# Optimization experiments

Hardware: AMD Instinct MI355X
Metric: run time of the kernel (lower is better)

Reference implementation:

```python
import jax, jax.numpy as jnp
import numpy as np

T, D, I, E, K = 2048, 768, 2048, 8, 2


def setup_inputs() -> dict:
    key = jax.random.key(0)
    ks = jax.random.split(key, 9)
    x = jax.random.normal(ks[0], (T, D), jnp.float32)
    router_weight = jax.random.normal(ks[1], (E, D), jnp.float32) * 0.02
    shared_w_gate = jax.random.normal(ks[2], (I, D), jnp.float32) * 0.02
    shared_w_up = jax.random.normal(ks[3], (I, D), jnp.float32) * 0.02
    shared_w_down = jax.random.normal(ks[4], (D, I), jnp.float32) * 0.02
    # ternary quantized expert weights in {-1, 0, 1}
    expert_q_gate = jax.random.randint(ks[5], (E, I, D), 0, 3, jnp.int32) - 1
    expert_q_up = jax.random.randint(ks[6], (E, I, D), 0, 3, jnp.int32) - 1
    expert_q_down = jax.random.randint(ks[7], (E, D, I), 0, 3, jnp.int32) - 1
    # per-expert, per-matrix dequant scales (gate, up, down)
    expert_scales = jax.random.uniform(ks[8], (E, 3), jnp.float32) * 0.05 + 0.01
    return {
        "x": x,
        "router_weight": router_weight,
        "shared_w_gate": shared_w_gate,
        "shared_w_up": shared_w_up,
        "shared_w_down": shared_w_down,
        "expert_q_gate": expert_q_gate,
        "expert_q_up": expert_q_up,
        "expert_q_down": expert_q_down,
        "expert_scales": expert_scales,
        "top_k": K,
    }


def _swiglu(x, wg, wu, wd):
    # down( silu(gate(x)) * up(x) )
    return (jax.nn.silu(x @ wg.T) * (x @ wu.T)) @ wd.T


def reference(x, router_weight, shared_w_gate, shared_w_up, shared_w_down,
              expert_q_gate, expert_q_up, expert_q_down, expert_scales, top_k):
    # --- router: softmax -> top-k -> renormalize ---
    probs = jax.nn.softmax(x @ router_weight.T, axis=-1)            # [T, E]
    vals, idx = jax.lax.top_k(probs, top_k)                          # [T, K]
    vals = vals / jnp.sum(vals, axis=-1, keepdims=True)
    n_experts = router_weight.shape[0]
    # combine weights as dense [T, E] gate (one-hot scatter of top-k probs)
    gate = jnp.sum(jax.nn.one_hot(idx, n_experts, dtype=x.dtype) * vals[..., None], axis=1)

    # --- dequantize paged ternary experts: w = ternary * scale ---
    wg = expert_q_gate.astype(x.dtype) * expert_scales[:, 0, None, None]  # [E, I, D]
    wu = expert_q_up.astype(x.dtype) * expert_scales[:, 1, None, None]    # [E, I, D]
    wd = expert_q_down.astype(x.dtype) * expert_scales[:, 2, None, None]  # [E, D, I]

    # --- expert SwiGLU, computed per expert and combined with the gate ---
    h = jax.nn.silu(jnp.einsum('td,eid->tei', x, wg)) * jnp.einsum('td,eid->tei', x, wu)
    expert_out = jnp.einsum('tei,edi->ted', h, wd)                   # [T, E, D]
    moe_out = jnp.einsum('te,ted->td', gate, expert_out)             # [T, D]

    # --- always-on shared expert ---
    shared_out = _swiglu(x, shared_w_gate, shared_w_up, shared_w_down)
    return shared_out + moe_out
```

## Files before the change

### kernel.cpp

```cpp
#include <hip/hip_runtime.h>
#include <hip/hip_bf16.h>

#define TDIM 2048
#define DDIM 768
#define IDIM 2048
#define NEXP 8

typedef __bf16 v8bf __attribute__((ext_vector_type(8)));
typedef __bf16 v4bf __attribute__((ext_vector_type(4)));
typedef float v4f __attribute__((ext_vector_type(4)));
typedef int   v4i __attribute__((ext_vector_type(4)));
typedef float v4ff __attribute__((ext_vector_type(4)));

#define MFMA_B16(A,B,C) __builtin_amdgcn_mfma_f32_16x16x32_bf16(A,B,C,0,0,0)

typedef __attribute__((address_space(1))) const unsigned int* gas_t;
typedef __attribute__((address_space(3))) unsigned int* las_t;

__device__ __forceinline__ void gload16(const void* g, void* l) {
  __builtin_amdgcn_global_load_lds((gas_t)g, (las_t)l, 16, 0, 0);
}

__device__ __forceinline__ v4bf cvt4_i(v4i a) {
  v4bf v;
  v[0] = (__bf16)(float)a[0]; v[1] = (__bf16)(float)a[1];
  v[2] = (__bf16)(float)a[2]; v[3] = (__bf16)(float)a[3];
  return v;
}
__device__ __forceinline__ v4bf cvt4_f(v4ff a) {
  v4bf v;
  v[0] = (__bf16)a[0]; v[1] = (__bf16)a[1]; v[2] = (__bf16)a[2]; v[3] = (__bf16)a[3];
  return v;
}

__global__ __launch_bounds__(256)
void pack_all_kernel(const int* __restrict__ qg, const int* __restrict__ qu,
                     const int* __restrict__ qd,
                     const float* __restrict__ sg, const float* __restrict__ su,
                     const float* __restrict__ sd, const float* __restrict__ x,
                     const float* __restrict__ rw, const float* __restrict__ es,
                     __hip_bfloat16* __restrict__ wguT, __hip_bfloat16* __restrict__ sguT,
                     __hip_bfloat16* __restrict__ wdT,  __hip_bfloat16* __restrict__ sdT,
                     __hip_bfloat16* __restrict__ xb,
                     int* __restrict__ cnt, int* __restrict__ lists, float* __restrict__ wt)
{
  const int b = blockIdx.x;
  const int tid = threadIdx.x;

  if (b < 512) {
    const int t = b * 4 + (tid >> 6);
    const int lane = tid & 63;
    const float* xp = x + (size_t)t * DDIM;
    float4 xv0 = *(const float4*)(xp + lane * 4);
    float4 xv1 = *(const float4*)(xp + 256 + lane * 4);
    float4 xv2 = *(const float4*)(xp + 512 + lane * 4);
    float logit[NEXP];
#pragma unroll
    for (int e = 0; e < NEXP; ++e) {
      const float* w = rw + (size_t)e * DDIM;
      float4 w0 = *(const float4*)(w + lane * 4);
      float4 w1 = *(const float4*)(w + 256 + lane * 4);
      float4 w2 = *(const float4*)(w + 512 + lane * 4);
      float p = xv0.x * w0.x + xv0.y * w0.y + xv0.z * w0.z + xv0.w * w0.w
              + xv1.x * w1.x + xv1.y * w1.y + xv1.z * w1.z + xv1.w * w1.w
              + xv2.x * w2.x + xv2.y * w2.y + xv2.z * w2.z + xv2.w * w2.w;
#pragma unroll
      for (int off = 32; off > 0; off >>= 1) p += __shfl_down(p, off, 64);
      logit[e] = p;
    }
    if (lane == 0) {
      float m = logit[0];
#pragma unroll
      for (int e = 1; e < NEXP; ++e) m = fmaxf(m, logit[e]);
      float pr[NEXP];
#pragma unroll
      for (int e = 0; e < NEXP; ++e) pr[e] = expf(logit[e] - m);
      int i0 = 0; float v0 = pr[0];
#pragma unroll
      for (int e = 1; e < NEXP; ++e) if (pr[e] > v0) { v0 = pr[e]; i0 = e; }
      int i1 = -1; float v1 = -1.f;
#pragma unroll
      for (int e = 0; e < NEXP; ++e) if (e != i0 && pr[e] > v1) { v1 = pr[e]; i1 = e; }
      float inv = 1.f / (v0 + v1);
      int p0 = atomicAdd(&cnt[i0], 1);
      lists[i0 * TDIM + p0] = t * 2;
      wt[t * 2] = v0 * inv * es[i0 * 3 + 2];
      int p1 = atomicAdd(&cnt[i1], 1);
      lists[i1 * TDIM + p1] = t * 2 + 1;
      wt[t * 2 + 1] = v1 * inv * es[i1 * 3 + 2];
    }
    return;
  }

  const int lc = tid & 31;
  const int rowloc = tid >> 5;

  if (b < 768) {
    const int row = (b - 512) * 8 + rowloc;
    const float* sp = x + (size_t)row * DDIM;
    __hip_bfloat16* dp = xb + (size_t)row * DDIM;
    v4ff r[6];
#pragma unroll
    for (int i = 0; i < 6; ++i) r[i] = *(const v4ff*)(sp + (lc + i * 32) * 4);
#pragma unroll
    for (int i = 0; i < 6; ++i) *(v4bf*)(dp + (lc + i * 32) * 4) = cvt4_f(r[i]);
    return;
  }

  if (b < 5376) {
    const int pb = b - 768;
    const int* isrc = nullptr; const float* fsrc = nullptr;
    char* dstT; int T, r8, isint;
    if (pb < 4096) {
      const int e = pb >> 9; T = (pb >> 8) & 1; r8 = pb & 255;
      isrc = (T ? qu : qg) + (size_t)e * IDIM * DDIM;
      dstT = (char*)wguT + (size_t)e * 32 * 12 * 16384;
      isint = 1;
    } else {
      const int sb = pb - 4096; T = sb >> 8; r8 = sb & 255;
      fsrc = T ? su : sg;
      dstT = (char*)sguT;
      isint = 0;
    }
    const int srcrow = r8 * 8 + rowloc;
    const int rg = ((srcrow >> 4) * 32) + (srcrow & 15) + T * 16;
    const int tnt = rg >> 7, rowin = rg & 127;
    const int xorm = (rowin & 7) << 4;
    char* rowdst = dstT + (size_t)tnt * (12 * 16384) + rowin * 128;
    const size_t soff = (size_t)srcrow * DDIM;

    if (isint) {
      v4i r[6];
#pragma unroll
      for (int i = 0; i < 6; ++i) r[i] = *(const v4i*)(isrc + soff + (lc + i * 32) * 4);
#pragma unroll
      for (int i = 0; i < 6; ++i) {
        const int c4 = lc + i * 32;
        const int kt = c4 >> 4;
        *(v4bf*)(rowdst + (size_t)kt * 16384 + (((c4 & 15) << 3) ^ xorm)) = cvt4_i(r[i]);
      }
    } else {
      v4ff r[6];
#pragma unroll
      for (int i = 0; i < 6; ++i) r[i] = *(const v4ff*)(fsrc + soff + (lc + i * 32) * 4);
#pragma unroll
      for (int i = 0; i < 6; ++i) {
        const int c4 = lc + i * 32;
        const int kt = c4 >> 4;
        *(v4bf*)(rowdst + (size_t)kt * 16384 + (((c4 & 15) << 3) ^ xorm)) = cvt4_f(r[i]);
      }
    }
    return;
  }

  {
    const int pb = b - 5376;
    const int* isrc = nullptr; const float* fsrc = nullptr;
    char* dstT; int r8, isint;
    if (pb < 768) {
      const int e = pb / 96; r8 = pb % 96;
      isrc = qd + (size_t)e * DDIM * IDIM;
      dstT = (char*)wdT + (size_t)e * (192 * 16384);
      isint = 1;
    } else {
      r8 = pb - 768;
      fsrc = sd;
      dstT = (char*)sdT;
      isint = 0;
    }
    const int srcrow = r8 * 8 + rowloc;
    const int tnt = srcrow >> 7, rowin = srcrow & 127;
    const int xorm = (rowin & 7) << 4;
    char* rowdst = dstT + (size_t)tnt * (32 * 16384) + rowin * 128;
    const size_t soff = (size_t)srcrow * IDIM;

#pragma unroll
    for (int h = 0; h < 2; ++h) {
      if (isint) {
        v4i r[8];
#pragma unroll
        for (int j = 0; j < 8; ++j) r[j] = *(const v4i*)(isrc + soff + (lc + (h * 8 + j) * 32) * 4);
#pragma unroll
        for (int j = 0; j < 8; ++j) {
          const int c4 = lc + (h * 8 + j) * 32;
          const int kt = c4 >> 4;
          *(v4bf*)(rowdst + (size_t)kt * 16384 + (((c4 & 15) << 3) ^ xorm)) = cvt4_i(r[j]);
        }
      } else {
        v4ff r[8];
#pragma unroll
        for (int j = 0; j < 8; ++j) r[j] = *(const v4ff*)(fsrc + soff + (lc + (h * 8 + j) * 32) * 4);
#pragma unroll
        for (int j = 0; j < 8; ++j) {
          const int c4 = lc + (h * 8 + j) * 32;
          const int kt = c4 >> 4;
          *(v4bf*)(rowdst + (size_t)kt * 16384 + (((c4 & 15) << 3) ^ xorm)) = cvt4_f(r[j]);
        }
      }
    }
  }
}

__global__ __launch_bounds__(256, 3)
void gu_gemm_kernel(const __hip_bfloat16* __restrict__ xb,
                    const __hip_bfloat16* __restrict__ wguT, const __hip_bfloat16* __restrict__ sguT,
                    const float* __restrict__ es,
                    const int* __restrict__ cnt, const int* __restrict__ lists,
                    __hip_bfloat16* __restrict__ h)
{
  const int b = blockIdx.x;
  int tm, tn, count;
  const char* bbase;
  const int* listE = nullptr;
  float sgc, suc;
  if (b < 4096) {
    const int e = b >> 9; tm = (b >> 5) & 15; tn = b & 31;
    count = cnt[e];
    if (tm * 128 >= count) return;
    bbase = (const char*)wguT + (size_t)(e * 32 + tn) * (12 * 16384);
    listE = lists + e * TDIM;
    sgc = es[e * 3 + 0]; suc = es[e * 3 + 1];
  } else {
    const int b2 = b - 4096; tm = b2 >> 5; tn = b2 & 31;
    count = TDIM;
    bbase = (const char*)sguT + (size_t)tn * (12 * 16384);
    sgc = 1.f; suc = 1.f;
  }

  __shared__ __align__(16) char As[16384];
  __shared__ __align__(16) char Bs[16384];

  const int tid = threadIdx.x;
  const int lane = tid & 63;
  const int wid = tid >> 6;
  const int wr = wid >> 1, wc = wid & 1;
  const int lr16 = lane & 15, hk = lane >> 4;

  const int cA = (((lane & 7) ^ (lane >> 3)) << 4);
  const char* aptr[4];
#pragma unroll
  for (int p = 0; p < 4; ++p) {
    const int row = p * 32 + wid * 8 + (lane >> 3);
    const int rg = tm * 128 + row;
    int tok;
    if (listE) { const int idx = rg < count ? rg : count - 1; tok = listE[idx] >> 1; }
    else tok = rg;
    aptr[p] = (const char*)xb + (size_t)tok * (DDIM * 2) + cA;
  }
  const char* bp = bbase + wid * 1024 + lane * 16;

  v4f acc[4][4] = {};

  for (int kt = 0; kt < 12; ++kt) {
#pragma unroll
    for (int p = 0; p < 4; ++p) gload16(aptr[p] + kt * 128, As + wid * 1024 + p * 4096);
#pragma unroll
    for (int p = 0; p < 4; ++p) gload16(bp + kt * 16384 + p * 4096, Bs + wid * 1024 + p * 4096);
    __syncthreads();
#pragma unroll
    for (int ks = 0; ks < 2; ++ks) {
      const int colb = ks * 64 + hk * 16;
      v8bf fa[4], fb[4];
#pragma unroll
      for (int m = 0; m < 4; ++m) {
        const int r = wr * 64 + m * 16 + lr16;
        fa[m] = *(const v8bf*)(As + r * 128 + (colb ^ ((r & 7) << 4)));
      }
#pragma unroll
      for (int n = 0; n < 4; ++n) {
        const int r = wc * 64 + n * 16 + lr16;
        fb[n] = *(const v8bf*)(Bs + r * 128 + (colb ^ ((r & 7) << 4)));
      }
#pragma unroll
      for (int n = 0; n < 4; ++n)
#pragma unroll
        for (int m = 0; m < 4; ++m) acc[m][n] = MFMA_B16(fa[m], fb[n], acc[m][n]);
    }
    __syncthreads();
  }

#pragma unroll
  for (int m = 0; m < 4; ++m) {
#pragma unroll
    for (int j = 0; j < 4; ++j) {
      const int rl = wr * 64 + m * 16 + hk * 4 + j;
      const int rg = tm * 128 + rl;
      if (rg >= count) continue;
      const size_t drow = listE ? (size_t)listE[rg] : (size_t)(4096 + rg);
      __hip_bfloat16* dh = h + drow * IDIM + (tn * 4 + wc * 2) * 16 + lr16;
#pragma unroll
      for (int p = 0; p < 2; ++p) {
        const float g = acc[m][2 * p][j] * sgc;
        const float u = acc[m][2 * p + 1][j] * suc;
        dh[p * 16] = __float2bfloat16(g / (1.f + __expf(-g)) * u);
      }
    }
  }
}

__global__ __launch_bounds__(256, 3)
void down_kernel(const __hip_bfloat16* __restrict__ h,
                 const __hip_bfloat16* __restrict__ wdT, const __hip_bfloat16* __restrict__ sdT,
                 const float* __restrict__ wt,
                 const int* __restrict__ cnt, const int* __restrict__ lists,
                 float* __restrict__ out)
{
  const int b = blockIdx.x;
  int tm, tn, count;
  const char* bbase;
  const int* listE = nullptr;
  if (b < 768) {
    const int e = b / 96; const int r = b % 96; tm = r / 6; tn = r % 6;
    count = cnt[e];
    if (tm * 128 >= count) return;
    bbase = (const char*)wdT + (size_t)(e * 6 + tn) * (32 * 16384);
    listE = lists + e * TDIM;
  } else {
    const int r = b - 768; tm = r / 6; tn = r % 6;
    count = TDIM;
    bbase = (const char*)sdT + (size_t)tn * (32 * 16384);
  }

  __shared__ __align__(16) char As[16384];
  __shared__ __align__(16) char Bs[16384];

  const int tid = threadIdx.x;
  const int lane = tid & 63;
  const int wid = tid >> 6;
  const int wr = wid >> 1, wc = wid & 1;
  const int lr16 = lane & 15, hk = lane >> 4;

  const int cA = (((lane & 7) ^ (lane >> 3)) << 4);
  const char* aptr[4];
#pragma unroll
  for (int p = 0; p < 4; ++p) {
    const int row = p * 32 + wid * 8 + (lane >> 3);
    const int rg = tm * 128 + row;
    int srow;
    if (listE) { const int idx = rg < count ? rg : count - 1; srow = listE[idx]; }
    else srow = 4096 + rg;
    aptr[p] = (const char*)h + (size_t)srow * (IDIM * 2) + cA;
  }
  const char* bp = bbase + wid * 1024 + lane * 16;

  v4f acc[4][4] = {};

  for (int kt = 0; kt < 32; ++kt) {
#pragma unroll
    for (int p = 0; p < 4; ++p) gload16(aptr[p] + kt * 128, As + wid * 1024 + p * 4096);
#pragma unroll
    for (int p = 0; p < 4; ++p) gload16(bp + kt * 16384 + p * 4096, Bs + wid * 1024 + p * 4096);
    __syncthreads();
#pragma unroll
    for (int ks = 0; ks < 2; ++ks) {
      const int colb = ks * 64 + hk * 16;
      v8bf fa[4], fb[4];
#pragma unroll
      for (int m = 0; m < 4; ++m) {
        const int r = wr * 64 + m * 16 + lr16;
        fa[m] = *(const v8bf*)(As + r * 128 + (colb ^ ((r & 7) << 4)));
      }
#pragma unroll
      for (int n = 0; n < 4; ++n) {
        const int r = wc * 64 + n * 16 + lr16;
        fb[n] = *(const v8bf*)(Bs + r * 128 + (colb ^ ((r & 7) << 4)));
      }
#pragma unroll
      for (int n = 0; n < 4; ++n)
#pragma unroll
        for (int m = 0; m < 4; ++m) acc[m][n] = MFMA_B16(fa[m], fb[n], acc[m][n]);
    }
    __syncthreads();
  }

#pragma unroll
  for (int m = 0; m < 4; ++m) {
#pragma unroll
    for (int j = 0; j < 4; ++j) {
      const int rl = wr * 64 + m * 16 + hk * 4 + j;
      const int rg = tm * 128 + rl;
      if (rg >= count) continue;
      int tok; float w;
      if (listE) { const int slot = listE[rg]; tok = slot >> 1; w = wt[slot]; }
      else { tok = rg; w = 1.f; }
      float* dst = out + (size_t)tok * DDIM + tn * 128 + wc * 64 + lr16;
#pragma unroll
      for (int n = 0; n < 4; ++n) atomicAdd(dst + n * 16, acc[m][n][j] * w);
    }
  }
}

extern "C" void kernel_launch(void* const* d_in, const int* in_sizes, int n_in,
                              void* d_out, int out_size, void* d_ws, size_t ws_size,
                              hipStream_t stream)
{
  const float* x   = (const float*)d_in[0];
  const float* rw  = (const float*)d_in[1];
  const float* swg = (const float*)d_in[2];
  const float* swu = (const float*)d_in[3];
  const float* swd = (const float*)d_in[4];
  const int*   qg  = (const int*)d_in[5];
  const int*   qu  = (const int*)d_in[6];
  const int*   qd  = (const int*)d_in[7];
  const float* es  = (const float*)d_in[8];
  float* out = (float*)d_out;

  char* ws = (char*)d_ws;
  size_t off = 0;
  auto alloc = [&](size_t bytes) { void* p = ws + off; off = (off + bytes + 255) & ~(size_t)255; return p; };
  int*   cnt   = (int*)alloc(NEXP * 4);
  int*   lists = (int*)alloc((size_t)NEXP * TDIM * 4);
  float* wt    = (float*)alloc((size_t)2 * TDIM * 4);
  __hip_bfloat16* xb   = (__hip_bfloat16*)alloc((size_t)TDIM * DDIM * 2);
  __hip_bfloat16* wguT = (__hip_bfloat16*)alloc((size_t)NEXP * 32 * 12 * 8192 * 2);
  __hip_bfloat16* sguT = (__hip_bfloat16*)alloc((size_t)32 * 12 * 8192 * 2);
  __hip_bfloat16* wdT  = (__hip_bfloat16*)alloc((size_t)NEXP * 6 * 32 * 8192 * 2);
  __hip_bfloat16* sdT  = (__hip_bfloat16*)alloc((size_t)6 * 32 * 8192 * 2);
  __hip_bfloat16* h    = (__hip_bfloat16*)alloc((size_t)(4096 + TDIM) * IDIM * 2);

  hipMemsetAsync(cnt, 0, NEXP * 4, stream);
  hipMemsetAsync(out, 0, (size_t)TDIM * DDIM * 4, stream);

  pack_all_kernel<<<6240, 256, 0, stream>>>(qg, qu, qd, swg, swu, swd, x, rw, es,
                                            wguT, sguT, wdT, sdT, xb, cnt, lists, wt);
  gu_gemm_kernel<<<4096 + 512, 256, 0, stream>>>(xb, wguT, sguT, es, cnt, lists, h);
  down_kernel<<<768 + 96, 256, 0, stream>>>(h, wdT, sdT, wt, cnt, lists, out);
}
```

Baseline: 351.4 us.

## Fuse weight dequantization into GEMM loads and replace atomics with combine pass

Drops the separate pack pass that converted int32 ternary and fp32 shared weights into pre-swizzled bf16 buffers. The GEMM kernels now read the raw weights, convert them in registers and store them to LDS, with register prefetch and a double-buffered A tile. The down kernel writes per-slot partial outputs rather than doing atomicAdd into out, and a new combine kernel sums the two expert partials and the shared partial for each token. This avoids a large write and re-read of packed weights, but each GEMM tile now re-reads 4-byte weights (twice the bf16 bytes) and does the conversion every time, and the combine pass adds extra traffic.

```diff
diff --git a/kernel.cpp b/kernel.cpp
--- a/kernel.cpp
+++ b/kernel.cpp
@@ -21,28 +21,22 @@
   __builtin_amdgcn_global_load_lds((gas_t)g, (las_t)l, 16, 0, 0);
 }
 
-__device__ __forceinline__ v4bf cvt4_i(v4i a) {
+__device__ __forceinline__ v4bf conv4(v4i r, int isint) {
   v4bf v;
-  v[0] = (__bf16)(float)a[0]; v[1] = (__bf16)(float)a[1];
-  v[2] = (__bf16)(float)a[2]; v[3] = (__bf16)(float)a[3];
+  if (isint) {
+    v[0] = (__bf16)(float)r[0]; v[1] = (__bf16)(float)r[1];
+    v[2] = (__bf16)(float)r[2]; v[3] = (__bf16)(float)r[3];
+  } else {
+    v[0] = (__bf16)__int_as_float(r[0]); v[1] = (__bf16)__int_as_float(r[1]);
+    v[2] = (__bf16)__int_as_float(r[2]); v[3] = (__bf16)__int_as_float(r[3]);
+  }
   return v;
 }
-__device__ __forceinline__ v4bf cvt4_f(v4ff a) {
-  v4bf v;
-  v[0] = (__bf16)a[0]; v[1] = (__bf16)a[1]; v[2] = (__bf16)a[2]; v[3] = (__bf16)a[3];
-  return v;
-}
 
 __global__ __launch_bounds__(256)
-void pack_all_kernel(const int* __restrict__ qg, const int* __restrict__ qu,
-                     const int* __restrict__ qd,
-                     const float* __restrict__ sg, const float* __restrict__ su,
-                     const float* __restrict__ sd, const float* __restrict__ x,
-                     const float* __restrict__ rw, const float* __restrict__ es,
-                     __hip_bfloat16* __restrict__ wguT, __hip_bfloat16* __restrict__ sguT,
-                     __hip_bfloat16* __restrict__ wdT,  __hip_bfloat16* __restrict__ sdT,
-                     __hip_bfloat16* __restrict__ xb,
-                     int* __restrict__ cnt, int* __restrict__ lists, float* __restrict__ wt)
+void prep_kernel(const float* __restrict__ x, const float* __restrict__ rw,
+                 const float* __restrict__ es, __hip_bfloat16* __restrict__ xb,
+                 int* __restrict__ cnt, int* __restrict__ lists, float* __restrict__ wt)
 {
   const int b = blockIdx.x;
   const int tid = threadIdx.x;
@@ -94,140 +88,51 @@
 
   const int lc = tid & 31;
   const int rowloc = tid >> 5;
-
-  if (b < 768) {
-    const int row = (b - 512) * 8 + rowloc;
-    const float* sp = x + (size_t)row * DDIM;
-    __hip_bfloat16* dp = xb + (size_t)row * DDIM;
-    v4ff r[6];
-#pragma unroll
-    for (int i = 0; i < 6; ++i) r[i] = *(const v4ff*)(sp + (lc + i * 32) * 4);
-#pragma unroll
-    for (int i = 0; i < 6; ++i) *(v4bf*)(dp + (lc + i * 32) * 4) = cvt4_f(r[i]);
-    return;
-  }
-
-  if (b < 5376) {
-    const int pb = b - 768;
-    const int* isrc = nullptr; const float* fsrc = nullptr;
-    char* dstT; int T, r8, isint;
-    if (pb < 4096) {
-      const int e = pb >> 9; T = (pb >> 8) & 1; r8 = pb & 255;
-      isrc = (T ? qu : qg) + (size_t)e * IDIM * DDIM;
-      dstT = (char*)wguT + (size_t)e * 32 * 12 * 16384;
-      isint = 1;
-    } else {
-      const int sb = pb - 4096; T = sb >> 8; r8 = sb & 255;
-      fsrc = T ? su : sg;
-      dstT = (char*)sguT;
-      isint = 0;
-    }
-    const int srcrow = r8 * 8 + rowloc;
-    const int rg = ((srcrow >> 4) * 32) + (srcrow & 15) + T * 16;
-    const int tnt = rg >> 7, rowin = rg & 127;
-    const int xorm = (rowin & 7) << 4;
-    char* rowdst = dstT + (size_t)tnt * (12 * 16384) + rowin * 128;
-    const size_t soff = (size_t)srcrow * DDIM;
-
-    if (isint) {
-      v4i r[6];
-#pragma unroll
-      for (int i = 0; i < 6; ++i) r[i] = *(const v4i*)(isrc + soff + (lc + i * 32) * 4);
-#pragma unroll
-      for (int i = 0; i < 6; ++i) {
-        const int c4 = lc + i * 32;
-        const int kt = c4 >> 4;
-        *(v4bf*)(rowdst + (size_t)kt * 16384 + (((c4 & 15) << 3) ^ xorm)) = cvt4_i(r[i]);
-      }
-    } else {
-      v4ff r[6];
-#pragma unroll
-      for (int i = 0; i < 6; ++i) r[i] = *(const v4ff*)(fsrc + soff + (lc + i * 32) * 4);
-#pragma unroll
-      for (int i = 0; i < 6; ++i) {
-        const int c4 = lc + i * 32;
-        const int kt = c4 >> 4;
-        *(v4bf*)(rowdst + (size_t)kt * 16384 + (((c4 & 15) << 3) ^ xorm)) = cvt4_f(r[i]);
-      }
-    }
-    return;
-  }
-
-  {
-    const int pb = b - 5376;
-    const int* isrc = nullptr; const float* fsrc = nullptr;
-    char* dstT; int r8, isint;
-    if (pb < 768) {
-      const int e = pb / 96; r8 = pb % 96;
-      isrc = qd + (size_t)e * DDIM * IDIM;
-      dstT = (char*)wdT + (size_t)e * (192 * 16384);
-      isint = 1;
-    } else {
-      r8 = pb - 768;
-      fsrc = sd;
-      dstT = (char*)sdT;
-      isint = 0;
-    }
-    const int srcrow = r8 * 8 + rowloc;
-    const int tnt = srcrow >> 7, rowin = srcrow & 127;
-    const int xorm = (rowin & 7) << 4;
-    char* rowdst = dstT + (size_t)tnt * (32 * 16384) + rowin * 128;
-    const size_t soff = (size_t)srcrow * IDIM;
-
-#pragma unroll
-    for (int h = 0; h < 2; ++h) {
-      if (isint) {
-        v4i r[8];
-#pragma unroll
-        for (int j = 0; j < 8; ++j) r[j] = *(const v4i*)(isrc + soff + (lc + (h * 8 + j) * 32) * 4);
-#pragma unroll
-        for (int j = 0; j < 8; ++j) {
-          const int c4 = lc + (h * 8 + j) * 32;
-          const int kt = c4 >> 4;
-          *(v4bf*)(rowdst + (size_t)kt * 16384 + (((c4 & 15) << 3) ^ xorm)) = cvt4_i(r[j]);
-        }
-      } else {
-        v4ff r[8];
-#pragma unroll
-        for (int j = 0; j < 8; ++j) r[j] = *(const v4ff*)(fsrc + soff + (lc + (h * 8 + j) * 32) * 4);
-#pragma unroll
-        for (int j = 0; j < 8; ++j) {
-          const int c4 = lc + (h * 8 + j) * 32;
-          const int kt = c4 >> 4;
-          *(v4bf*)(rowdst + (size_t)kt * 16384 + (((c4 & 15) << 3) ^ xorm)) = cvt4_f(r[j]);
-        }
-      }
-    }
-  }
-}
-
-__global__ __launch_bounds__(256, 3)
+  const int row = (b - 512) * 8 + rowloc;
+  const float* sp = x + (size_t)row * DDIM;
+  __hip_bfloat16* dp = xb + (size_t)row * DDIM;
+  v4ff r[6];
+#pragma unroll
+  for (int i = 0; i < 6; ++i) r[i] = *(const v4ff*)(sp + (lc + i * 32) * 4);
+#pragma unroll
+  for (int i = 0; i < 6; ++i) {
+    v4bf v;
+    v[0] = (__bf16)r[i][0]; v[1] = (__bf16)r[i][1];
+    v[2] = (__bf16)r[i][2]; v[3] = (__bf16)r[i][3];
+    *(v4bf*)(dp + (lc + i * 32) * 4) = v;
+  }
+}
+
+__global__ __launch_bounds__(256)
 void gu_gemm_kernel(const __hip_bfloat16* __restrict__ xb,
-                    const __hip_bfloat16* __restrict__ wguT, const __hip_bfloat16* __restrict__ sguT,
+                    const int* __restrict__ qg, const int* __restrict__ qu,
+                    const float* __restrict__ sgw, const float* __restrict__ suw,
                     const float* __restrict__ es,
                     const int* __restrict__ cnt, const int* __restrict__ lists,
                     __hip_bfloat16* __restrict__ h)
 {
   const int b = blockIdx.x;
-  int tm, tn, count;
-  const char* bbase;
+  int tm, tn, count, isint;
+  const char *srcG, *srcU;
   const int* listE = nullptr;
   float sgc, suc;
   if (b < 4096) {
     const int e = b >> 9; tm = (b >> 5) & 15; tn = b & 31;
     count = cnt[e];
     if (tm * 128 >= count) return;
-    bbase = (const char*)wguT + (size_t)(e * 32 + tn) * (12 * 16384);
+    srcG = (const char*)(qg + (size_t)e * IDIM * DDIM);
+    srcU = (const char*)(qu + (size_t)e * IDIM * DDIM);
     listE = lists + e * TDIM;
     sgc = es[e * 3 + 0]; suc = es[e * 3 + 1];
+    isint = 1;
   } else {
     const int b2 = b - 4096; tm = b2 >> 5; tn = b2 & 31;
     count = TDIM;
-    bbase = (const char*)sguT + (size_t)tn * (12 * 16384);
-    sgc = 1.f; suc = 1.f;
-  }
-
-  __shared__ __align__(16) char As[16384];
+    srcG = (const char*)sgw; srcU = (const char*)suw;
+    sgc = 1.f; suc = 1.f; isint = 0;
+  }
+
+  __shared__ __align__(16) char As[2][16384];
   __shared__ __align__(16) char Bs[16384];
 
   const int tid = threadIdx.x;
@@ -247,16 +152,42 @@
     else tok = rg;
     aptr[p] = (const char*)xb + (size_t)tok * (DDIM * 2) + cA;
   }
-  const char* bp = bbase + wid * 1024 + lane * 16;
+
+  const int lanec = tid & 15;
+  const int rowb = tid >> 4;
+  const char* bq[8];
+  int dsoff[8];
+#pragma unroll
+  for (int p = 0; p < 8; ++p) {
+    const int srcrow = (tn * 4 + (p >> 1)) * 16 + rowb;
+    const char* base = (p & 1) ? srcU : srcG;
+    bq[p] = base + ((size_t)srcrow * DDIM + lanec * 4) * 4;
+    const int r = rowb + 16 * p;
+    dsoff[p] = r * 128 + ((lanec * 8) ^ ((rowb & 7) << 4));
+  }
 
   v4f acc[4][4] = {};
+  v4i braw[8];
+  v4bf bconv[8];
+
+#pragma unroll
+  for (int p = 0; p < 4; ++p) gload16(aptr[p], As[0] + wid * 1024 + p * 4096);
+#pragma unroll
+  for (int p = 0; p < 8; ++p) braw[p] = *(const v4i*)(bq[p]);
+#pragma unroll
+  for (int p = 0; p < 8; ++p) bconv[p] = conv4(braw[p], isint);
 
   for (int kt = 0; kt < 12; ++kt) {
-#pragma unroll
-    for (int p = 0; p < 4; ++p) gload16(aptr[p] + kt * 128, As + wid * 1024 + p * 4096);
-#pragma unroll
-    for (int p = 0; p < 4; ++p) gload16(bp + kt * 16384 + p * 4096, Bs + wid * 1024 + p * 4096);
+    const int cur = kt & 1;
+#pragma unroll
+    for (int p = 0; p < 8; ++p) *(v4bf*)(Bs + dsoff[p]) = bconv[p];
     __syncthreads();
+    if (kt + 1 < 12) {
+#pragma unroll
+      for (int p = 0; p < 4; ++p) gload16(aptr[p] + (kt + 1) * 128, As[cur ^ 1] + wid * 1024 + p * 4096);
+#pragma unroll
+      for (int p = 0; p < 8; ++p) braw[p] = *(const v4i*)(bq[p] + (kt + 1) * 256);
+    }
 #pragma unroll
     for (int ks = 0; ks < 2; ++ks) {
       const int colb = ks * 64 + hk * 16;
@@ -264,7 +195,7 @@
 #pragma unroll
       for (int m = 0; m < 4; ++m) {
         const int r = wr * 64 + m * 16 + lr16;
-        fa[m] = *(const v8bf*)(As + r * 128 + (colb ^ ((r & 7) << 4)));
+        fa[m] = *(const v8bf*)(As[cur] + r * 128 + (colb ^ ((r & 7) << 4)));
       }
 #pragma unroll
       for (int n = 0; n < 4; ++n) {
@@ -277,6 +208,10 @@
         for (int m = 0; m < 4; ++m) acc[m][n] = MFMA_B16(fa[m], fb[n], acc[m][n]);
     }
     __syncthreads();
+    if (kt + 1 < 12) {
+#pragma unroll
+      for (int p = 0; p < 8; ++p) bconv[p] = conv4(braw[p], isint);
+    }
   }
 
 #pragma unroll
@@ -298,30 +233,32 @@
   }
 }
 
-__global__ __launch_bounds__(256, 3)
-void down_kernel(const __hip_bfloat16* __restrict__ h,
-                 const __hip_bfloat16* __restrict__ wdT, const __hip_bfloat16* __restrict__ sdT,
-                 const float* __restrict__ wt,
-                 const int* __restrict__ cnt, const int* __restrict__ lists,
-                 float* __restrict__ out)
+__global__ __launch_bounds__(256)
+void down_gemm_kernel(const __hip_bfloat16* __restrict__ h,
+                      const int* __restrict__ qd, const float* __restrict__ sdw,
+                      const float* __restrict__ wt,
+                      const int* __restrict__ cnt, const int* __restrict__ lists,
+                      float* __restrict__ part)
 {
   const int b = blockIdx.x;
-  int tm, tn, count;
-  const char* bbase;
+  int tm, tn, count, isint;
+  const char* srcB;
   const int* listE = nullptr;
   if (b < 768) {
     const int e = b / 96; const int r = b % 96; tm = r / 6; tn = r % 6;
     count = cnt[e];
     if (tm * 128 >= count) return;
-    bbase = (const char*)wdT + (size_t)(e * 6 + tn) * (32 * 16384);
+    srcB = (const char*)(qd + (size_t)e * DDIM * IDIM);
     listE = lists + e * TDIM;
+    isint = 1;
   } else {
     const int r = b - 768; tm = r / 6; tn = r % 6;
     count = TDIM;
-    bbase = (const char*)sdT + (size_t)tn * (32 * 16384);
-  }
-
-  __shared__ __align__(16) char As[16384];
+    srcB = (const char*)sdw;
+    isint = 0;
+  }
+
+  __shared__ __align__(16) char As[2][16384];
   __shared__ __align__(16) char Bs[16384];
 
   const int tid = threadIdx.x;
@@ -341,16 +278,41 @@
     else srow = 4096 + rg;
     aptr[p] = (const char*)h + (size_t)srow * (IDIM * 2) + cA;
   }
-  const char* bp = bbase + wid * 1024 + lane * 16;
+
+  const int lanec = tid & 15;
+  const int rowb = tid >> 4;
+  const char* bq[8];
+  int dsoff[8];
+#pragma unroll
+  for (int p = 0; p < 8; ++p) {
+    const int srcrow = tn * 128 + rowb + 16 * p;
+    bq[p] = srcB + ((size_t)srcrow * IDIM + lanec * 4) * 4;
+    const int r = rowb + 16 * p;
+    dsoff[p] = r * 128 + ((lanec * 8) ^ ((rowb & 7) << 4));
+  }
 
   v4f acc[4][4] = {};
+  v4i braw[8];
+  v4bf bconv[8];
+
+#pragma unroll
+  for (int p = 0; p < 4; ++p) gload16(aptr[p], As[0] + wid * 1024 + p * 4096);
+#pragma unroll
+  for (int p = 0; p < 8; ++p) braw[p] = *(const v4i*)(bq[p]);
+#pragma unroll
+  for (int p = 0; p < 8; ++p) bconv[p] = conv4(braw[p], isint);
 
   for (int kt = 0; kt < 32; ++kt) {
-#pragma unroll
-    for (int p = 0; p < 4; ++p) gload16(aptr[p] + kt * 128, As + wid * 1024 + p * 4096);
-#pragma unroll
-    for (int p = 0; p < 4; ++p) gload16(bp + kt * 16384 + p * 4096, Bs + wid * 1024 + p * 4096);
+    const int cur = kt & 1;
+#pragma unroll
+    for (int p = 0; p < 8; ++p) *(v4bf*)(Bs + dsoff[p]) = bconv[p];
     __syncthreads();
+    if (kt + 1 < 32) {
+#pragma unroll
+      for (int p = 0; p < 4; ++p) gload16(aptr[p] + (kt + 1) * 128, As[cur ^ 1] + wid * 1024 + p * 4096);
+#pragma unroll
+      for (int p = 0; p < 8; ++p) braw[p] = *(const v4i*)(bq[p] + (kt + 1) * 256);
+    }
 #pragma unroll
     for (int ks = 0; ks < 2; ++ks) {
       const int colb = ks * 64 + hk * 16;
@@ -358,7 +320,7 @@
 #pragma unroll
       for (int m = 0; m < 4; ++m) {
         const int r = wr * 64 + m * 16 + lr16;
-        fa[m] = *(const v8bf*)(As + r * 128 + (colb ^ ((r & 7) << 4)));
+        fa[m] = *(const v8bf*)(As[cur] + r * 128 + (colb ^ ((r & 7) << 4)));
       }
 #pragma unroll
       for (int n = 0; n < 4; ++n) {
@@ -371,6 +333,10 @@
         for (int m = 0; m < 4; ++m) acc[m][n] = MFMA_B16(fa[m], fb[n], acc[m][n]);
     }
     __syncthreads();
+    if (kt + 1 < 32) {
+#pragma unroll
+      for (int p = 0; p < 8; ++p) bconv[p] = conv4(braw[p], isint);
+    }
   }
 
 #pragma unroll
@@ -380,14 +346,32 @@
       const int rl = wr * 64 + m * 16 + hk * 4 + j;
       const int rg = tm * 128 + rl;
       if (rg >= count) continue;
-      int tok; float w;
-      if (listE) { const int slot = listE[rg]; tok = slot >> 1; w = wt[slot]; }
-      else { tok = rg; w = 1.f; }
-      float* dst = out + (size_t)tok * DDIM + tn * 128 + wc * 64 + lr16;
-#pragma unroll
-      for (int n = 0; n < 4; ++n) atomicAdd(dst + n * 16, acc[m][n][j] * w);
-    }
-  }
+      int orow; float w;
+      if (listE) { const int slot = listE[rg]; orow = slot; w = wt[slot]; }
+      else { orow = 4096 + rg; w = 1.f; }
+      float* dst = part + (size_t)orow * DDIM + tn * 128 + wc * 64 + lr16;
+#pragma unroll
+      for (int n = 0; n < 4; ++n) dst[n * 16] = acc[m][n][j] * w;
+    }
+  }
+}
+
+__global__ __launch_bounds__(256)
+void combine_kernel(const float* __restrict__ part, float* __restrict__ out)
+{
+  const int i4 = blockIdx.x * 256 + threadIdx.x;
+  const int i0 = i4 * 4;
+  const int t = i0 / DDIM;
+  const int d = i0 - t * DDIM;
+  float4 a = *(const float4*)(part + (size_t)(2 * t) * DDIM + d);
+  float4 bb = *(const float4*)(part + (size_t)(2 * t + 1) * DDIM + d);
+  float4 c = *(const float4*)(part + (size_t)(4096 + t) * DDIM + d);
+  float4 r;
+  r.x = a.x + bb.x + c.x;
+  r.y = a.y + bb.y + c.y;
+  r.z = a.z + bb.z + c.z;
+  r.w = a.w + bb.w + c.w;
+  *(float4*)(out + i0) = r;
 }
 
 extern "C" void kernel_launch(void* const* d_in, const int* in_sizes, int n_in,
@@ -411,18 +395,14 @@
   int*   cnt   = (int*)alloc(NEXP * 4);
   int*   lists = (int*)alloc((size_t)NEXP * TDIM * 4);
   float* wt    = (float*)alloc((size_t)2 * TDIM * 4);
-  __hip_bfloat16* xb   = (__hip_bfloat16*)alloc((size_t)TDIM * DDIM * 2);
-  __hip_bfloat16* wguT = (__hip_bfloat16*)alloc((size_t)NEXP * 32 * 12 * 8192 * 2);
-  __hip_bfloat16* sguT = (__hip_bfloat16*)alloc((size_t)32 * 12 * 8192 * 2);
-  __hip_bfloat16* wdT  = (__hip_bfloat16*)alloc((size_t)NEXP * 6 * 32 * 8192 * 2);
-  __hip_bfloat16* sdT  = (__hip_bfloat16*)alloc((size_t)6 * 32 * 8192 * 2);
-  __hip_bfloat16* h    = (__hip_bfloat16*)alloc((size_t)(4096 + TDIM) * IDIM * 2);
+  __hip_bfloat16* xb = (__hip_bfloat16*)alloc((size_t)TDIM * DDIM * 2);
+  __hip_bfloat16* h  = (__hip_bfloat16*)alloc((size_t)(4096 + TDIM) * IDIM * 2);
+  float* part = (float*)alloc((size_t)(4096 + TDIM) * DDIM * 4);
 
   hipMemsetAsync(cnt, 0, NEXP * 4, stream);
-  hipMemsetAsync(out, 0, (size_t)TDIM * DDIM * 4, stream);
-
-  pack_all_kernel<<<6240, 256, 0, stream>>>(qg, qu, qd, swg, swu, swd, x, rw, es,
-                                            wguT, sguT, wdT, sdT, xb, cnt, lists, wt);
-  gu_gemm_kernel<<<4096 + 512, 256, 0, stream>>>(xb, wguT, sguT, es, cnt, lists, h);
-  down_kernel<<<768 + 96, 256, 0, stream>>>(h, wdT, sdT, wt, cnt, lists, out);
-}
+
+  prep_kernel<<<768, 256, 0, stream>>>(x, rw, es, xb, cnt, lists, wt);
+  gu_gemm_kernel<<<4096 + 512, 256, 0, stream>>>(xb, qg, qu, swg, swu, es, cnt, lists, h);
+  down_gemm_kernel<<<768 + 96, 256, 0, stream>>>(h, qd, swd, wt, cnt, lists, part);
+  combine_kernel<<<(TDIM * DDIM / 4) / 256, 256, 0, stream>>>(part, out);
+}
```

Result: slower. 389.1 us (+10.7%).

## Store packed weights row-major and replace down atomics with partials plus combine

Applied to the files above, without the earlier changes.

The weight packing now writes plain row-major bf16 rows instead of pre-swizzled tile blocks. The GEMMs gather B rows with per-row pointers and an XOR column offset, which moves the swizzle from the pack stores to the load side. The down GEMM no longer does float atomicAdd into the output. It writes per-slot partial rows into a scratch buffer, and a new combine kernel sums the two expert slots and the shared row per token. This removes atomic contention and the output memset, at the cost of an extra kernel, extra scratch traffic, and strided B loads that are less contiguous.

```diff
diff --git a/kernel.cpp b/kernel.cpp
--- a/kernel.cpp
+++ b/kernel.cpp
@@ -39,8 +39,8 @@
                      const float* __restrict__ sg, const float* __restrict__ su,
                      const float* __restrict__ sd, const float* __restrict__ x,
                      const float* __restrict__ rw, const float* __restrict__ es,
-                     __hip_bfloat16* __restrict__ wguT, __hip_bfloat16* __restrict__ sguT,
-                     __hip_bfloat16* __restrict__ wdT,  __hip_bfloat16* __restrict__ sdT,
+                     __hip_bfloat16* __restrict__ wgub, __hip_bfloat16* __restrict__ sgub,
+                     __hip_bfloat16* __restrict__ wdb,  __hip_bfloat16* __restrict__ sdb,
                      __hip_bfloat16* __restrict__ xb,
                      int* __restrict__ cnt, int* __restrict__ lists, float* __restrict__ wt)
 {
@@ -110,45 +110,36 @@
   if (b < 5376) {
     const int pb = b - 768;
     const int* isrc = nullptr; const float* fsrc = nullptr;
-    char* dstT; int T, r8, isint;
+    __hip_bfloat16* dstT; int T, r8, isint;
     if (pb < 4096) {
       const int e = pb >> 9; T = (pb >> 8) & 1; r8 = pb & 255;
       isrc = (T ? qu : qg) + (size_t)e * IDIM * DDIM;
-      dstT = (char*)wguT + (size_t)e * 32 * 12 * 16384;
+      dstT = wgub + (size_t)e * (2 * IDIM) * DDIM;
       isint = 1;
     } else {
       const int sb = pb - 4096; T = sb >> 8; r8 = sb & 255;
       fsrc = T ? su : sg;
-      dstT = (char*)sguT;
+      dstT = sgub;
       isint = 0;
     }
     const int srcrow = r8 * 8 + rowloc;
     const int rg = ((srcrow >> 4) * 32) + (srcrow & 15) + T * 16;
-    const int tnt = rg >> 7, rowin = rg & 127;
-    const int xorm = (rowin & 7) << 4;
-    char* rowdst = dstT + (size_t)tnt * (12 * 16384) + rowin * 128;
-    const size_t soff = (size_t)srcrow * DDIM;
+    __hip_bfloat16* dp = dstT + (size_t)rg * DDIM;
 
     if (isint) {
+      const v4i* sp = (const v4i*)(isrc + (size_t)srcrow * DDIM);
       v4i r[6];
 #pragma unroll
-      for (int i = 0; i < 6; ++i) r[i] = *(const v4i*)(isrc + soff + (lc + i * 32) * 4);
-#pragma unroll
-      for (int i = 0; i < 6; ++i) {
-        const int c4 = lc + i * 32;
-        const int kt = c4 >> 4;
-        *(v4bf*)(rowdst + (size_t)kt * 16384 + (((c4 & 15) << 3) ^ xorm)) = cvt4_i(r[i]);
-      }
+      for (int i = 0; i < 6; ++i) r[i] = sp[lc + i * 32];
+#pragma unroll
+      for (int i = 0; i < 6; ++i) *(v4bf*)(dp + (lc + i * 32) * 4) = cvt4_i(r[i]);
     } else {
+      const v4ff* sp = (const v4ff*)(fsrc + (size_t)srcrow * DDIM);
       v4ff r[6];
 #pragma unroll
-      for (int i = 0; i < 6; ++i) r[i] = *(const v4ff*)(fsrc + soff + (lc + i * 32) * 4);
-#pragma unroll
-      for (int i = 0; i < 6; ++i) {
-        const int c4 = lc + i * 32;
-        const int kt = c4 >> 4;
-        *(v4bf*)(rowdst + (size_t)kt * 16384 + (((c4 & 15) << 3) ^ xorm)) = cvt4_f(r[i]);
-      }
+      for (int i = 0; i < 6; ++i) r[i] = sp[lc + i * 32];
+#pragma unroll
+      for (int i = 0; i < 6; ++i) *(v4bf*)(dp + (lc + i * 32) * 4) = cvt4_f(r[i]);
     }
     return;
   }
@@ -156,46 +147,37 @@
   {
     const int pb = b - 5376;
     const int* isrc = nullptr; const float* fsrc = nullptr;
-    char* dstT; int r8, isint;
+    __hip_bfloat16* dstT; int r8, isint;
     if (pb < 768) {
       const int e = pb / 96; r8 = pb % 96;
       isrc = qd + (size_t)e * DDIM * IDIM;
-      dstT = (char*)wdT + (size_t)e * (192 * 16384);
+      dstT = wdb + (size_t)e * DDIM * IDIM;
       isint = 1;
     } else {
       r8 = pb - 768;
       fsrc = sd;
-      dstT = (char*)sdT;
+      dstT = sdb;
       isint = 0;
     }
     const int srcrow = r8 * 8 + rowloc;
-    const int tnt = srcrow >> 7, rowin = srcrow & 127;
-    const int xorm = (rowin & 7) << 4;
-    char* rowdst = dstT + (size_t)tnt * (32 * 16384) + rowin * 128;
-    const size_t soff = (size_t)srcrow * IDIM;
-
-#pragma unroll
-    for (int h = 0; h < 2; ++h) {
+    __hip_bfloat16* dp = dstT + (size_t)srcrow * IDIM;
+
+#pragma unroll
+    for (int h2 = 0; h2 < 2; ++h2) {
       if (isint) {
+        const v4i* sp = (const v4i*)(isrc + (size_t)srcrow * IDIM);
         v4i r[8];
 #pragma unroll
-        for (int j = 0; j < 8; ++j) r[j] = *(const v4i*)(isrc + soff + (lc + (h * 8 + j) * 32) * 4);
-#pragma unroll
-        for (int j = 0; j < 8; ++j) {
-          const int c4 = lc + (h * 8 + j) * 32;
-          const int kt = c4 >> 4;
-          *(v4bf*)(rowdst + (size_t)kt * 16384 + (((c4 & 15) << 3) ^ xorm)) = cvt4_i(r[j]);
-        }
+        for (int j = 0; j < 8; ++j) r[j] = sp[lc + (h2 * 8 + j) * 32];
+#pragma unroll
+        for (int j = 0; j < 8; ++j) *(v4bf*)(dp + (lc + (h2 * 8 + j) * 32) * 4) = cvt4_i(r[j]);
       } else {
+        const v4ff* sp = (const v4ff*)(fsrc + (size_t)srcrow * IDIM);
         v4ff r[8];
 #pragma unroll
-        for (int j = 0; j < 8; ++j) r[j] = *(const v4ff*)(fsrc + soff + (lc + (h * 8 + j) * 32) * 4);
-#pragma unroll
-        for (int j = 0; j < 8; ++j) {
-          const int c4 = lc + (h * 8 + j) * 32;
-          const int kt = c4 >> 4;
-          *(v4bf*)(rowdst + (size_t)kt * 16384 + (((c4 & 15) << 3) ^ xorm)) = cvt4_f(r[j]);
-        }
+        for (int j = 0; j < 8; ++j) r[j] = sp[lc + (h2 * 8 + j) * 32];
+#pragma unroll
+        for (int j = 0; j < 8; ++j) *(v4bf*)(dp + (lc + (h2 * 8 + j) * 32) * 4) = cvt4_f(r[j]);
       }
     }
   }
@@ -203,7 +185,7 @@
 
 __global__ __launch_bounds__(256, 3)
 void gu_gemm_kernel(const __hip_bfloat16* __restrict__ xb,
-                    const __hip_bfloat16* __restrict__ wguT, const __hip_bfloat16* __restrict__ sguT,
+                    const __hip_bfloat16* __restrict__ wgub, const __hip_bfloat16* __restrict__ sgub,
                     const float* __restrict__ es,
                     const int* __restrict__ cnt, const int* __restrict__ lists,
                     __hip_bfloat16* __restrict__ h)
@@ -217,13 +199,13 @@
     const int e = b >> 9; tm = (b >> 5) & 15; tn = b & 31;
     count = cnt[e];
     if (tm * 128 >= count) return;
-    bbase = (const char*)wguT + (size_t)(e * 32 + tn) * (12 * 16384);
+    bbase = (const char*)(wgub + (size_t)e * (2 * IDIM) * DDIM);
     listE = lists + e * TDIM;
     sgc = es[e * 3 + 0]; suc = es[e * 3 + 1];
   } else {
     const int b2 = b - 4096; tm = b2 >> 5; tn = b2 & 31;
     count = TDIM;
-    bbase = (const char*)sguT + (size_t)tn * (12 * 16384);
+    bbase = (const char*)sgub;
     sgc = 1.f; suc = 1.f;
   }
 
@@ -238,6 +220,7 @@
 
   const int cA = (((lane & 7) ^ (lane >> 3)) << 4);
   const char* aptr[4];
+  const char* bptr[4];
 #pragma unroll
   for (int p = 0; p < 4; ++p) {
     const int row = p * 32 + wid * 8 + (lane >> 3);
@@ -246,8 +229,8 @@
     if (listE) { const int idx = rg < count ? rg : count - 1; tok = listE[idx] >> 1; }
     else tok = rg;
     aptr[p] = (const char*)xb + (size_t)tok * (DDIM * 2) + cA;
-  }
-  const char* bp = bbase + wid * 1024 + lane * 16;
+    bptr[p] = bbase + (size_t)(tn * 128 + row) * (DDIM * 2) + cA;
+  }
 
   v4f acc[4][4] = {};
 
@@ -255,7 +238,7 @@
 #pragma unroll
     for (int p = 0; p < 4; ++p) gload16(aptr[p] + kt * 128, As + wid * 1024 + p * 4096);
 #pragma unroll
-    for (int p = 0; p < 4; ++p) gload16(bp + kt * 16384 + p * 4096, Bs + wid * 1024 + p * 4096);
+    for (int p = 0; p < 4; ++p) gload16(bptr[p] + kt * 128, Bs + wid * 1024 + p * 4096);
     __syncthreads();
 #pragma unroll
     for (int ks = 0; ks < 2; ++ks) {
@@ -299,11 +282,11 @@
 }
 
 __global__ __launch_bounds__(256, 3)
-void down_kernel(const __hip_bfloat16* __restrict__ h,
-                 const __hip_bfloat16* __restrict__ wdT, const __hip_bfloat16* __restrict__ sdT,
-                 const float* __restrict__ wt,
-                 const int* __restrict__ cnt, const int* __restrict__ lists,
-                 float* __restrict__ out)
+void down_gemm_kernel(const __hip_bfloat16* __restrict__ h,
+                      const __hip_bfloat16* __restrict__ wdb, const __hip_bfloat16* __restrict__ sdb,
+                      const float* __restrict__ wt,
+                      const int* __restrict__ cnt, const int* __restrict__ lists,
+                      float* __restrict__ part)
 {
   const int b = blockIdx.x;
   int tm, tn, count;
@@ -313,12 +296,12 @@
     const int e = b / 96; const int r = b % 96; tm = r / 6; tn = r % 6;
     count = cnt[e];
     if (tm * 128 >= count) return;
-    bbase = (const char*)wdT + (size_t)(e * 6 + tn) * (32 * 16384);
+    bbase = (const char*)(wdb + (size_t)e * DDIM * IDIM);
     listE = lists + e * TDIM;
   } else {
     const int r = b - 768; tm = r / 6; tn = r % 6;
     count = TDIM;
-    bbase = (const char*)sdT + (size_t)tn * (32 * 16384);
+    bbase = (const char*)sdb;
   }
 
   __shared__ __align__(16) char As[16384];
@@ -332,6 +315,7 @@
 
   const int cA = (((lane & 7) ^ (lane >> 3)) << 4);
   const char* aptr[4];
+  const char* bptr[4];
 #pragma unroll
   for (int p = 0; p < 4; ++p) {
     const int row = p * 32 + wid * 8 + (lane >> 3);
@@ -340,8 +324,8 @@
     if (listE) { const int idx = rg < count ? rg : count - 1; srow = listE[idx]; }
     else srow = 4096 + rg;
     aptr[p] = (const char*)h + (size_t)srow * (IDIM * 2) + cA;
-  }
-  const char* bp = bbase + wid * 1024 + lane * 16;
+    bptr[p] = bbase + (size_t)(tn * 128 + row) * (IDIM * 2) + cA;
+  }
 
   v4f acc[4][4] = {};
 
@@ -349,7 +333,7 @@
 #pragma unroll
     for (int p = 0; p < 4; ++p) gload16(aptr[p] + kt * 128, As + wid * 1024 + p * 4096);
 #pragma unroll
-    for (int p = 0; p < 4; ++p) gload16(bp + kt * 16384 + p * 4096, Bs + wid * 1024 + p * 4096);
+    for (int p = 0; p < 4; ++p) gload16(bptr[p] + kt * 128, Bs + wid * 1024 + p * 4096);
     __syncthreads();
 #pragma unroll
     for (int ks = 0; ks < 2; ++ks) {
@@ -380,14 +364,32 @@
       const int rl = wr * 64 + m * 16 + hk * 4 + j;
       const int rg = tm * 128 + rl;
       if (rg >= count) continue;
-      int tok; float w;
-      if (listE) { const int slot = listE[rg]; tok = slot >> 1; w = wt[slot]; }
-      else { tok = rg; w = 1.f; }
-      float* dst = out + (size_t)tok * DDIM + tn * 128 + wc * 64 + lr16;
-#pragma unroll
-      for (int n = 0; n < 4; ++n) atomicAdd(dst + n * 16, acc[m][n][j] * w);
-    }
-  }
+      int orow; float w;
+      if (listE) { const int slot = listE[rg]; orow = slot; w = wt[slot]; }
+      else { orow = 4096 + rg; w = 1.f; }
+      float* dst = part + (size_t)orow * DDIM + tn * 128 + wc * 64 + lr16;
+#pragma unroll
+      for (int n = 0; n < 4; ++n) dst[n * 16] = acc[m][n][j] * w;
+    }
+  }
+}
+
+__global__ __launch_bounds__(256)
+void combine_kernel(const float* __restrict__ part, float* __restrict__ out)
+{
+  const int i4 = blockIdx.x * 256 + threadIdx.x;
+  const int i0 = i4 * 4;
+  const int t = i0 / DDIM;
+  const int d = i0 - t * DDIM;
+  float4 a = *(const float4*)(part + (size_t)(2 * t) * DDIM + d);
+  float4 bb = *(const float4*)(part + (size_t)(2 * t + 1) * DDIM + d);
+  float4 c = *(const float4*)(part + (size_t)(4096 + t) * DDIM + d);
+  float4 r;
+  r.x = a.x + bb.x + c.x;
+  r.y = a.y + bb.y + c.y;
+  r.z = a.z + bb.z + c.z;
+  r.w = a.w + bb.w + c.w;
+  *(float4*)(out + i0) = r;
 }
 
 extern "C" void kernel_launch(void* const* d_in, const int* in_sizes, int n_in,
@@ -412,17 +414,18 @@
   int*   lists = (int*)alloc((size_t)NEXP * TDIM * 4);
   float* wt    = (float*)alloc((size_t)2 * TDIM * 4);
   __hip_bfloat16* xb   = (__hip_bfloat16*)alloc((size_t)TDIM * DDIM * 2);
-  __hip_bfloat16* wguT = (__hip_bfloat16*)alloc((size_t)NEXP * 32 * 12 * 8192 * 2);
-  __hip_bfloat16* sguT = (__hip_bfloat16*)alloc((size_t)32 * 12 * 8192 * 2);
-  __hip_bfloat16* wdT  = (__hip_bfloat16*)alloc((size_t)NEXP * 6 * 32 * 8192 * 2);
-  __hip_bfloat16* sdT  = (__hip_bfloat16*)alloc((size_t)6 * 32 * 8192 * 2);
+  __hip_bfloat16* wgub = (__hip_bfloat16*)alloc((size_t)NEXP * 2 * IDIM * DDIM * 2);
+  __hip_bfloat16* sgub = (__hip_bfloat16*)alloc((size_t)2 * IDIM * DDIM * 2);
+  __hip_bfloat16* wdb  = (__hip_bfloat16*)alloc((size_t)NEXP * DDIM * IDIM * 2);
+  __hip_bfloat16* sdb  = (__hip_bfloat16*)alloc((size_t)DDIM * IDIM * 2);
   __hip_bfloat16* h    = (__hip_bfloat16*)alloc((size_t)(4096 + TDIM) * IDIM * 2);
+  float* part = (float*)alloc((size_t)(4096 + TDIM) * DDIM * 4);
 
   hipMemsetAsync(cnt, 0, NEXP * 4, stream);
-  hipMemsetAsync(out, 0, (size_t)TDIM * DDIM * 4, stream);
 
   pack_all_kernel<<<6240, 256, 0, stream>>>(qg, qu, qd, swg, swu, swd, x, rw, es,
-                                            wguT, sguT, wdT, sdT, xb, cnt, lists, wt);
-  gu_gemm_kernel<<<4096 + 512, 256, 0, stream>>>(xb, wguT, sguT, es, cnt, lists, h);
-  down_kernel<<<768 + 96, 256, 0, stream>>>(h, wdT, sdT, wt, cnt, lists, out);
-}
+                                            wgub, sgub, wdb, sdb, xb, cnt, lists, wt);
+  gu_gemm_kernel<<<4096 + 512, 256, 0, stream>>>(xb, wgub, sgub, es, cnt, lists, h);
+  down_gemm_kernel<<<768 + 96, 256, 0, stream>>>(h, wdb, sdb, wt, cnt, lists, part);
+  combine_kernel<<<(TDIM * DDIM / 4) / 256, 256, 0, stream>>>(part, out);
+}
```

Result: faster. 343.8 us (-2.1%).
